# Kernel optimization log

Hardware: AMD Instinct MI355X
Metric: run time of the kernel (lower is better)

Reference implementation:

```python
import jax, jax.numpy as jnp
import numpy as np

N = 4096        # nodes
IN_DIM = 256    # input feature dim
HID = 64        # hidden per head (num_hidden_layers)
HEADS = 8
OUT_DIM = 64
ALPHA = 0.2     # LeakyReLU negative slope
NEG_INF = jnp.float32(-9e15)


def setup_inputs() -> dict:
    key = jax.random.key(0)
    ks = jax.random.split(key, 8)
    x = jax.random.normal(ks[0], (N, IN_DIM), dtype=jnp.float32)
    adj = (jax.random.uniform(ks[1], (N, N)) < 0.002).astype(jnp.float32)
    adj = jnp.maximum(adj, jnp.eye(N, dtype=jnp.float32))
    s = 0.1
    W_h = jax.random.normal(ks[2], (HEADS, IN_DIM, HID), dtype=jnp.float32) * s
    a1_h = jax.random.normal(ks[3], (HEADS, HID), dtype=jnp.float32) * s
    a2_h = jax.random.normal(ks[4], (HEADS, HID), dtype=jnp.float32) * s
    W_o = jax.random.normal(ks[5], (HEADS * HID, OUT_DIM), dtype=jnp.float32) * s
    a1_o = jax.random.normal(ks[6], (OUT_DIM,), dtype=jnp.float32) * s
    a2_o = jax.random.normal(ks[7], (OUT_DIM,), dtype=jnp.float32) * s
    return dict(x=x, adj=adj, W_h=W_h, a1_h=a1_h, a2_h=a2_h, W_o=W_o, a1_o=a1_o, a2_o=a2_o)


def _gat_heads(x, adj, W, a1, a2):
    """Multi-head GAT layer. x:[N,F], adj:[N,N], W:[H,F,O], a1/a2:[H,O] -> [H,N,O]."""
    Wh = jnp.einsum('nf,hfo->hno', x, W)                      # [H,N,O]
    f1 = jnp.einsum('hno,ho->hn', Wh, a1)                     # source scores
    f2 = jnp.einsum('hno,ho->hn', Wh, a2)                     # target scores
    e = jax.nn.leaky_relu(f1[:, :, None] + f2[:, None, :], ALPHA)  # [H,N,N]
    e = jnp.where(adj[None] > 0, e, NEG_INF)
    attn = jax.nn.softmax(e, axis=-1)                         # segment-softmax over neighbors
    return jnp.einsum('hnm,hmo->hno', attn, Wh)


def reference(x, adj, W_h, a1_h, a2_h, W_o, a1_o, a2_o):
    # dropout p=0.0 -> identity (deterministic reference)
    h = _gat_heads(x, adj, W_h, a1_h, a2_h)                   # [H,N,HID]
    h = jnp.transpose(h, (1, 0, 2)).reshape(N, HEADS * HID)   # concat heads on dim=-1
    out = _gat_heads(h, adj, W_o[None], a1_o[None], a2_o[None])[0]  # [N,OUT_DIM]
    return jax.nn.elu(out)
```

## Files before the change

kernel.cpp:

```cpp
#include <hip/hip_runtime.h>
#include <cstdint>
#include <cstddef>

#define N_NODES 4096
#define IN_DIM 256
#define HID 64
#define HEADS 8
#define OUT_DIM 64
#define ALPHA 0.2f
#define MAXDEG 64
#define TILE 16

typedef __attribute__((ext_vector_type(8))) short bf16x8;
typedef __attribute__((ext_vector_type(4))) float f32x4;

__device__ __forceinline__ unsigned short f2bf(float f) {
    unsigned u = __float_as_uint(f);
    u += 0x7fffu + ((u >> 16) & 1u);
    return (unsigned short)(u >> 16);
}
__device__ __forceinline__ float bf2f(unsigned short u) {
    return __uint_as_float(((unsigned)u) << 16);
}

__global__ __launch_bounds__(256) void k1_gemm_csr(const float* __restrict__ x,
                                                   const float* __restrict__ W,
                                                   const float* __restrict__ a1,
                                                   const float* __restrict__ a2,
                                                   unsigned short* __restrict__ Whb,
                                                   float* __restrict__ f1,
                                                   float* __restrict__ f2,
                                                   const float* __restrict__ adj,
                                                   int* __restrict__ degs,
                                                   int* __restrict__ cols) {
    __shared__ __attribute__((aligned(16))) unsigned short axs[64][72];
    __shared__ __attribute__((aligned(16))) unsigned short bws[64][72];
    int bid = blockIdx.x;
    int t = threadIdx.x;
    int w = t >> 6, l = t & 63;
    if (bid % 9 == 0) {
        int g = bid / 9;
        int h = g & 7;
        int n0 = (g >> 3) * 64;
        int m0 = (w >> 1) * 32;
        int np = (w & 1) * 32;
        f32x4 zf = {0.f, 0.f, 0.f, 0.f};
        f32x4 acc[2][2] = {{zf, zf}, {zf, zf}};
        const float4* x4 = (const float4*)x;
        const float4* w4 = (const float4*)(W + (size_t)h * IN_DIM * HID);
        for (int kc = 0; kc < IN_DIM; kc += 64) {
            __syncthreads();
            #pragma unroll
            for (int i = 0; i < 4; ++i) {
                int e = t + i * 256;
                int r = e >> 4, c4 = e & 15;
                float4 v = x4[(size_t)(n0 + r) * (IN_DIM / 4) + (kc >> 2) + c4];
                ushort4 u;
                u.x = f2bf(v.x); u.y = f2bf(v.y); u.z = f2bf(v.z); u.w = f2bf(v.w);
                *(ushort4*)&axs[r][c4 * 4] = u;
            }
            #pragma unroll
            for (int i = 0; i < 4; ++i) {
                int e = t + i * 256;
                int kk = e >> 4, c4 = e & 15;
                float4 v = w4[(size_t)(kc + kk) * (HID / 4) + c4];
                bws[4 * c4 + 0][kk] = f2bf(v.x);
                bws[4 * c4 + 1][kk] = f2bf(v.y);
                bws[4 * c4 + 2][kk] = f2bf(v.z);
                bws[4 * c4 + 3][kk] = f2bf(v.w);
            }
            __syncthreads();
            #pragma unroll
            for (int k0 = 0; k0 < 64; k0 += 32) {
                bf16x8 af[2], bfr[2];
                #pragma unroll
                for (int m = 0; m < 2; ++m)
                    af[m] = *(const bf16x8*)&axs[m0 + m * 16 + (l & 15)][k0 + (l >> 4) * 8];
                #pragma unroll
                for (int n = 0; n < 2; ++n)
                    bfr[n] = *(const bf16x8*)&bws[np + n * 16 + (l & 15)][k0 + (l >> 4) * 8];
                #pragma unroll
                for (int m = 0; m < 2; ++m)
                    #pragma unroll
                    for (int n = 0; n < 2; ++n)
                        acc[m][n] = __builtin_amdgcn_mfma_f32_16x16x32_bf16(af[m], bfr[n], acc[m][n], 0, 0, 0);
            }
        }
        __syncthreads();
        float a1c[2], a2c[2];
        #pragma unroll
        for (int n = 0; n < 2; ++n) {
            a1c[n] = a1[h * HID + np + n * 16 + (l & 15)];
            a2c[n] = a2[h * HID + np + n * 16 + (l & 15)];
        }
        float* fred = (float*)&axs[0][0];
        int wn = w & 1;
        #pragma unroll
        for (int m = 0; m < 2; ++m) {
            #pragma unroll
            for (int r = 0; r < 4; ++r) {
                int row = m0 + m * 16 + (l >> 4) * 4 + r;
                #pragma unroll
                for (int n = 0; n < 2; ++n)
                    Whb[((size_t)(n0 + row) * HEADS + h) * HID + np + n * 16 + (l & 15)] =
                        f2bf(acc[m][n][r]);
                float s1 = acc[m][0][r] * a1c[0] + acc[m][1][r] * a1c[1];
                float s2 = acc[m][0][r] * a2c[0] + acc[m][1][r] * a2c[1];
                #pragma unroll
                for (int off = 8; off; off >>= 1) {
                    s1 += __shfl_xor(s1, off);
                    s2 += __shfl_xor(s2, off);
                }
                if ((l & 15) == 0) {
                    fred[0 * 128 + wn * 64 + row] = s1;
                    fred[1 * 128 + wn * 64 + row] = s2;
                }
            }
        }
        __syncthreads();
        if (t < 64) {
            f1[(size_t)(n0 + t) * HEADS + h] = fred[t] + fred[64 + t];
            f2[(size_t)(n0 + t) * HEADS + h] = fred[128 + t] + fred[192 + t];
        }
    } else {
        int g = bid / 9, r9 = bid % 9;
        int row = g * 8 + r9 - 1;
        int* wcols = (int*)&axs[0][0];
        int* wcnt  = (int*)&bws[0][0];
        const float4* arow = (const float4*)(adj + (size_t)row * N_NODES);
        float4 v0 = arow[w * 256 + 0 * 64 + l];
        float4 v1 = arow[w * 256 + 1 * 64 + l];
        float4 v2 = arow[w * 256 + 2 * 64 + l];
        float4 v3 = arow[w * 256 + 3 * 64 + l];
        int base = 0;
        float4 vv[4] = {v0, v1, v2, v3};
        #pragma unroll
        for (int i = 0; i < 4; ++i) {
            float comp[4] = {vv[i].x, vv[i].y, vv[i].z, vv[i].w};
            #pragma unroll
            for (int q = 0; q < 4; ++q) {
                bool pred = comp[q] > 0.f;
                unsigned long long mask = __ballot(pred);
                if (pred) {
                    int pos = base + __popcll(mask & ((1ull << l) - 1ull));
                    if (pos < MAXDEG) wcols[w * MAXDEG + pos] = (w * 256 + i * 64 + l) * 4 + q;
                }
                base += __popcll(mask);
            }
        }
        if (l == 0) wcnt[w] = base < MAXDEG ? base : MAXDEG;
        __syncthreads();
        int c0 = wcnt[0], c1 = wcnt[1], c2 = wcnt[2], c3 = wcnt[3];
        int off = (w > 0 ? c0 : 0) + (w > 1 ? c1 : 0) + (w > 2 ? c2 : 0);
        int mycnt = wcnt[w];
        if (l < mycnt) {
            int gpos = off + l;
            if (gpos < MAXDEG) cols[row * MAXDEG + gpos] = wcols[w * MAXDEG + l];
        }
        if (t == 0) {
            int tot = c0 + c1 + c2 + c3;
            degs[row] = tot < MAXDEG ? tot : MAXDEG;
        }
    }
}

__global__ __launch_bounds__(256) void attn1_gemm2(const unsigned short* __restrict__ Whb,
                                                   const float* __restrict__ f1,
                                                   const float* __restrict__ f2,
                                                   const int* __restrict__ degs,
                                                   const int* __restrict__ cols,
                                                   const float* __restrict__ Wo,
                                                   const float* __restrict__ a1,
                                                   const float* __restrict__ a2,
                                                   float* __restrict__ Wh2,
                                                   float* __restrict__ f1o,
                                                   float* __restrict__ f2o) {
    __shared__ int   cols_s[TILE][MAXDEG];
    __shared__ int   deg_s[TILE];
    __shared__ float p_s[TILE][HEADS][MAXDEG];
    __shared__ __attribute__((aligned(16))) unsigned short htile[TILE][520];
    __shared__ __attribute__((aligned(16))) unsigned short bws[64][136];
    __shared__ float fred[2][4][TILE];

    int n0 = blockIdx.x * TILE;
    int t = threadIdx.x;
    int w = t >> 6, l = t & 63;

    if (t < TILE) deg_s[t] = degs[n0 + t];
    {
        int nl = t >> 4, ix = t & 15;
        #pragma unroll
        for (int it = 0; it < 4; ++it)
            cols_s[nl][ix + it * 16] = cols[(size_t)(n0 + nl) * MAXDEG + ix + it * 16];
    }
    __syncthreads();

    if (t < TILE * HEADS) {
        int nl = t >> 3, h = t & 7;
        int n = n0 + nl;
        int deg = deg_s[nl];
        float f1v = f1[n * HEADS + h];
        float m = -1e30f;
        for (int j = 0; j < deg; ++j) {
            int c = cols_s[nl][j];
            float v = f1v + f2[c * HEADS + h];
            v = v > 0.f ? v : ALPHA * v;
            p_s[nl][h][j] = v;
            m = fmaxf(m, v);
        }
        float s = 0.f;
        for (int j = 0; j < deg; ++j) {
            float p = expf(p_s[nl][h][j] - m);
            p_s[nl][h][j] = p;
            s += p;
        }
        float inv = 1.f / s;
        for (int j = 0; j < deg; ++j) p_s[nl][h][j] *= inv;
    }
    __syncthreads();

    {
        int nl = t >> 4, s16 = t & 15;
        int deg = deg_s[nl];
        float acc[4][8] = {};
        const uint4* whp = (const uint4*)Whb;
        for (int j = 0; j < deg; ++j) {
            int c = cols_s[nl][j];
            uint4 u[4];
            #pragma unroll
            for (int it = 0; it < 4; ++it)
                u[it] = whp[(size_t)c * 64 + it * 16 + s16];
            float pj[4];
            #pragma unroll
            for (int it = 0; it < 4; ++it) pj[it] = p_s[nl][it * 2 + (s16 >> 3)][j];
            #pragma unroll
            for (int it = 0; it < 4; ++it) {
                const unsigned short* up = (const unsigned short*)&u[it];
                #pragma unroll
                for (int q = 0; q < 8; ++q)
                    acc[it][q] += pj[it] * bf2f(up[q]);
            }
        }
        #pragma unroll
        for (int it = 0; it < 4; ++it) {
            unsigned short ov[8];
            #pragma unroll
            for (int q = 0; q < 8; ++q) ov[q] = f2bf(acc[it][q]);
            *(uint4*)&htile[nl][it * 128 + s16 * 8] = *(const uint4*)ov;
        }
    }

    f32x4 gacc = {0.f, 0.f, 0.f, 0.f};
    const float4* wo4 = (const float4*)Wo;
    int nbase = w * 16;
    for (int kc = 0; kc < HEADS * HID; kc += 128) {
        __syncthreads();
        #pragma unroll
        for (int i = 0; i < 8; ++i) {
            int e = t + i * 256;
            int kk = e >> 4, c4 = e & 15;
            float4 v = wo4[(size_t)(kc + kk) * (OUT_DIM / 4) + c4];
            bws[4 * c4 + 0][kk] = f2bf(v.x);
            bws[4 * c4 + 1][kk] = f2bf(v.y);
            bws[4 * c4 + 2][kk] = f2bf(v.z);
            bws[4 * c4 + 3][kk] = f2bf(v.w);
        }
        __syncthreads();
        #pragma unroll
        for (int k0 = 0; k0 < 128; k0 += 32) {
            bf16x8 af = *(const bf16x8*)&htile[l & 15][kc + k0 + (l >> 4) * 8];
            bf16x8 bfr = *(const bf16x8*)&bws[nbase + (l & 15)][k0 + (l >> 4) * 8];
            gacc = __builtin_amdgcn_mfma_f32_16x16x32_bf16(af, bfr, gacc, 0, 0, 0);
        }
    }
    float a1c = a1[nbase + (l & 15)];
    float a2c = a2[nbase + (l & 15)];
    #pragma unroll
    for (int r = 0; r < 4; ++r) {
        int row = (l >> 4) * 4 + r;
        Wh2[(size_t)(n0 + row) * OUT_DIM + nbase + (l & 15)] = gacc[r];
        float s1 = gacc[r] * a1c;
        float s2 = gacc[r] * a2c;
        #pragma unroll
        for (int off = 8; off; off >>= 1) {
            s1 += __shfl_xor(s1, off);
            s2 += __shfl_xor(s2, off);
        }
        if ((l & 15) == 0) {
            fred[0][w][row] = s1;
            fred[1][w][row] = s2;
        }
    }
    __syncthreads();
    if (t < TILE) {
        f1o[n0 + t] = fred[0][0][t] + fred[0][1][t] + fred[0][2][t] + fred[0][3][t];
        f2o[n0 + t] = fred[1][0][t] + fred[1][1][t] + fred[1][2][t] + fred[1][3][t];
    }
}

__global__ __launch_bounds__(256) void attn2(const float* __restrict__ Wh,
                                             const float* __restrict__ f1,
                                             const float* __restrict__ f2,
                                             const int* __restrict__ degs,
                                             const int* __restrict__ cols,
                                             float* __restrict__ out) {
    int wave = threadIdx.x >> 6;
    int lane = threadIdx.x & 63;
    int n = blockIdx.x * 4 + wave;
    if (n >= N_NODES) return;
    int deg = degs[n];
    int col = 0;
    float e = -1e30f;
    if (lane < deg) {
        col = cols[n * MAXDEG + lane];
        float v = f1[n] + f2[col];
        e = v > 0.f ? v : ALPHA * v;
    }
    float m = e;
    #pragma unroll
    for (int off = 32; off; off >>= 1) m = fmaxf(m, __shfl_xor(m, off));
    float p = (lane < deg) ? expf(e - m) : 0.f;
    float s = p;
    #pragma unroll
    for (int off = 32; off; off >>= 1) s += __shfl_xor(s, off);
    float inv = 1.f / s;
    float acc = 0.f;
    int j = 0;
    for (; j + 8 <= deg; j += 8) {
        int cj[8]; float pj[8]; float v[8];
        #pragma unroll
        for (int q = 0; q < 8; ++q) cj[q] = __shfl(col, j + q);
        #pragma unroll
        for (int q = 0; q < 8; ++q) pj[q] = __shfl(p, j + q);
        #pragma unroll
        for (int q = 0; q < 8; ++q) v[q] = Wh[(size_t)cj[q] * OUT_DIM + lane];
        #pragma unroll
        for (int q = 0; q < 8; ++q) acc += pj[q] * v[q];
    }
    for (; j < deg; ++j) {
        int cj = __shfl(col, j);
        float pj = __shfl(p, j);
        acc += pj * Wh[(size_t)cj * OUT_DIM + lane];
    }
    acc *= inv;
    acc = acc > 0.f ? acc : expf(acc) - 1.f;
    out[(size_t)n * OUT_DIM + lane] = acc;
}

extern "C" void kernel_launch(void* const* d_in, const int* in_sizes, int n_in,
                              void* d_out, int out_size, void* d_ws, size_t ws_size,
                              hipStream_t stream) {
    const float* x    = (const float*)d_in[0];
    const float* adj  = (const float*)d_in[1];
    const float* W_h  = (const float*)d_in[2];
    const float* a1_h = (const float*)d_in[3];
    const float* a2_h = (const float*)d_in[4];
    const float* W_o  = (const float*)d_in[5];
    const float* a1_o = (const float*)d_in[6];
    const float* a2_o = (const float*)d_in[7];
    float* out = (float*)d_out;

    float* wsf  = (float*)d_ws;
    float* Wh2  = wsf;
    float* f1_1 = Wh2 + (size_t)N_NODES * OUT_DIM;
    float* f2_1 = f1_1 + (size_t)N_NODES * HEADS;
    float* f1_2 = f2_1 + (size_t)N_NODES * HEADS;
    float* f2_2 = f1_2 + N_NODES;
    int*   degs = (int*)(f2_2 + N_NODES);
    int*   csr  = degs + N_NODES;
    unsigned short* Whb = (unsigned short*)(csr + (size_t)N_NODES * MAXDEG);

    k1_gemm_csr<<<4608, 256, 0, stream>>>(x, W_h, a1_h, a2_h, Whb, f1_1, f2_1, adj, degs, csr);

    attn1_gemm2<<<N_NODES / TILE, 256, 0, stream>>>(Whb, f1_1, f2_1, degs, csr,
                                                    W_o, a1_o, a2_o, Wh2, f1_2, f2_2);

    attn2<<<N_NODES / 4, 256, 0, stream>>>(Wh2, f1_2, f2_2, degs, csr, out);
}
```

Baseline: 53.07 us.

## Halve attn1 tile, pretranspose Wo to bf16 in k1, unroll neighbor loop

Moves the Wo fp32-to-bf16 transpose into 32 extra blocks of the first kernel, so each attn1 block copies ready bf16 rows into LDS instead of converting and scattering per block. The attn1 tile drops from 16 to 8 nodes, doubling the block count to 512 for better CU occupancy. The 8 padding rows of the MFMA A tile are zeroed and their outputs masked. The neighbor aggregation now uses 32 threads per node and unrolls two neighbors per iteration to raise memory-level parallelism. The cost is that each block reloads the full WoT for half as many nodes.

```diff
diff --git a/kernel.cpp b/kernel.cpp
--- a/kernel.cpp
+++ b/kernel.cpp
@@ -9,7 +9,7 @@
 #define OUT_DIM 64
 #define ALPHA 0.2f
 #define MAXDEG 64
-#define TILE 16
+#define TILE 8
 
 typedef __attribute__((ext_vector_type(8))) short bf16x8;
 typedef __attribute__((ext_vector_type(4))) float f32x4;
@@ -32,12 +32,25 @@
                                                    float* __restrict__ f2,
                                                    const float* __restrict__ adj,
                                                    int* __restrict__ degs,
-                                                   int* __restrict__ cols) {
+                                                   int* __restrict__ cols,
+                                                   const float* __restrict__ Wo,
+                                                   unsigned short* __restrict__ WoT) {
     __shared__ __attribute__((aligned(16))) unsigned short axs[64][72];
     __shared__ __attribute__((aligned(16))) unsigned short bws[64][72];
     int bid = blockIdx.x;
     int t = threadIdx.x;
     int w = t >> 6, l = t & 63;
+    if (bid >= 4608) {
+        int k0 = (bid - 4608) * 16;
+        #pragma unroll
+        for (int i = 0; i < 4; ++i) {
+            int e = t + i * 256;
+            int kk = k0 + (e >> 6);
+            int o = e & 63;
+            WoT[(size_t)o * 512 + kk] = f2bf(Wo[(size_t)kk * OUT_DIM + o]);
+        }
+        return;
+    }
     if (bid % 9 == 0) {
         int g = bid / 9;
         int h = g & 7;
@@ -169,7 +182,7 @@
                                                    const float* __restrict__ f2,
                                                    const int* __restrict__ degs,
                                                    const int* __restrict__ cols,
-                                                   const float* __restrict__ Wo,
+                                                   const unsigned short* __restrict__ WoT,
                                                    const float* __restrict__ a1,
                                                    const float* __restrict__ a2,
                                                    float* __restrict__ Wh2,
@@ -178,7 +191,7 @@
     __shared__ int   cols_s[TILE][MAXDEG];
     __shared__ int   deg_s[TILE];
     __shared__ float p_s[TILE][HEADS][MAXDEG];
-    __shared__ __attribute__((aligned(16))) unsigned short htile[TILE][520];
+    __shared__ __attribute__((aligned(16))) unsigned short htile[16][520];
     __shared__ __attribute__((aligned(16))) unsigned short bws[64][136];
     __shared__ float fred[2][4][TILE];
 
@@ -188,22 +201,29 @@
 
     if (t < TILE) deg_s[t] = degs[n0 + t];
     {
-        int nl = t >> 4, ix = t & 15;
-        #pragma unroll
-        for (int it = 0; it < 4; ++it)
-            cols_s[nl][ix + it * 16] = cols[(size_t)(n0 + nl) * MAXDEG + ix + it * 16];
+        int nl = t >> 5, ix = t & 31;
+        cols_s[nl][ix]      = cols[(size_t)(n0 + nl) * MAXDEG + ix];
+        cols_s[nl][ix + 32] = cols[(size_t)(n0 + nl) * MAXDEG + ix + 32];
+    }
+    {
+        uint4 z = {0u, 0u, 0u, 0u};
+        #pragma unroll
+        for (int i = 0; i < 2; ++i) {
+            int e = t + i * 256;
+            int r = 8 + (e >> 6), c8 = e & 63;
+            *(uint4*)&htile[r][c8 * 8] = z;
+        }
     }
     __syncthreads();
 
     if (t < TILE * HEADS) {
         int nl = t >> 3, h = t & 7;
-        int n = n0 + nl;
         int deg = deg_s[nl];
-        float f1v = f1[n * HEADS + h];
+        float f1v = f1[(size_t)(n0 + nl) * HEADS + h];
         float m = -1e30f;
         for (int j = 0; j < deg; ++j) {
             int c = cols_s[nl][j];
-            float v = f1v + f2[c * HEADS + h];
+            float v = f1v + f2[(size_t)c * HEADS + h];
             v = v > 0.f ? v : ALPHA * v;
             p_s[nl][h][j] = v;
             m = fmaxf(m, v);
@@ -220,50 +240,59 @@
     __syncthreads();
 
     {
-        int nl = t >> 4, s16 = t & 15;
+        int nl = t >> 5, s = t & 31;
         int deg = deg_s[nl];
-        float acc[4][8] = {};
+        int hA = s >> 3, hB = 4 + (s >> 3);
+        float accA[8] = {}, accB[8] = {};
         const uint4* whp = (const uint4*)Whb;
-        for (int j = 0; j < deg; ++j) {
-            int c = cols_s[nl][j];
-            uint4 u[4];
-            #pragma unroll
-            for (int it = 0; it < 4; ++it)
-                u[it] = whp[(size_t)c * 64 + it * 16 + s16];
-            float pj[4];
-            #pragma unroll
-            for (int it = 0; it < 4; ++it) pj[it] = p_s[nl][it * 2 + (s16 >> 3)][j];
-            #pragma unroll
-            for (int it = 0; it < 4; ++it) {
-                const unsigned short* up = (const unsigned short*)&u[it];
-                #pragma unroll
-                for (int q = 0; q < 8; ++q)
-                    acc[it][q] += pj[it] * bf2f(up[q]);
-            }
-        }
-        #pragma unroll
-        for (int it = 0; it < 4; ++it) {
-            unsigned short ov[8];
-            #pragma unroll
-            for (int q = 0; q < 8; ++q) ov[q] = f2bf(acc[it][q]);
-            *(uint4*)&htile[nl][it * 128 + s16 * 8] = *(const uint4*)ov;
-        }
+        int j = 0;
+        for (; j + 2 <= deg; j += 2) {
+            int c0 = cols_s[nl][j], c1 = cols_s[nl][j + 1];
+            uint4 u0a = whp[(size_t)c0 * 64 + s];
+            uint4 u0b = whp[(size_t)c0 * 64 + 32 + s];
+            uint4 u1a = whp[(size_t)c1 * 64 + s];
+            uint4 u1b = whp[(size_t)c1 * 64 + 32 + s];
+            float p0a = p_s[nl][hA][j],     p0b = p_s[nl][hB][j];
+            float p1a = p_s[nl][hA][j + 1], p1b = p_s[nl][hB][j + 1];
+            const unsigned short* w0a = (const unsigned short*)&u0a;
+            const unsigned short* w0b = (const unsigned short*)&u0b;
+            const unsigned short* w1a = (const unsigned short*)&u1a;
+            const unsigned short* w1b = (const unsigned short*)&u1b;
+            #pragma unroll
+            for (int q = 0; q < 8; ++q) {
+                accA[q] += p0a * bf2f(w0a[q]) + p1a * bf2f(w1a[q]);
+                accB[q] += p0b * bf2f(w0b[q]) + p1b * bf2f(w1b[q]);
+            }
+        }
+        if (j < deg) {
+            int c0 = cols_s[nl][j];
+            uint4 u0a = whp[(size_t)c0 * 64 + s];
+            uint4 u0b = whp[(size_t)c0 * 64 + 32 + s];
+            float p0a = p_s[nl][hA][j], p0b = p_s[nl][hB][j];
+            const unsigned short* w0a = (const unsigned short*)&u0a;
+            const unsigned short* w0b = (const unsigned short*)&u0b;
+            #pragma unroll
+            for (int q = 0; q < 8; ++q) {
+                accA[q] += p0a * bf2f(w0a[q]);
+                accB[q] += p0b * bf2f(w0b[q]);
+            }
+        }
+        unsigned short ovA[8], ovB[8];
+        #pragma unroll
+        for (int q = 0; q < 8; ++q) { ovA[q] = f2bf(accA[q]); ovB[q] = f2bf(accB[q]); }
+        *(uint4*)&htile[nl][s * 8]       = *(const uint4*)ovA;
+        *(uint4*)&htile[nl][256 + s * 8] = *(const uint4*)ovB;
     }
 
     f32x4 gacc = {0.f, 0.f, 0.f, 0.f};
-    const float4* wo4 = (const float4*)Wo;
     int nbase = w * 16;
     for (int kc = 0; kc < HEADS * HID; kc += 128) {
         __syncthreads();
         #pragma unroll
-        for (int i = 0; i < 8; ++i) {
+        for (int i = 0; i < 4; ++i) {
             int e = t + i * 256;
-            int kk = e >> 4, c4 = e & 15;
-            float4 v = wo4[(size_t)(kc + kk) * (OUT_DIM / 4) + c4];
-            bws[4 * c4 + 0][kk] = f2bf(v.x);
-            bws[4 * c4 + 1][kk] = f2bf(v.y);
-            bws[4 * c4 + 2][kk] = f2bf(v.z);
-            bws[4 * c4 + 3][kk] = f2bf(v.w);
+            int o = e >> 4, c8 = e & 15;
+            *(uint4*)&bws[o][c8 * 8] = *(const uint4*)&WoT[(size_t)o * 512 + kc + c8 * 8];
         }
         __syncthreads();
         #pragma unroll
@@ -278,7 +307,6 @@
     #pragma unroll
     for (int r = 0; r < 4; ++r) {
         int row = (l >> 4) * 4 + r;
-        Wh2[(size_t)(n0 + row) * OUT_DIM + nbase + (l & 15)] = gacc[r];
         float s1 = gacc[r] * a1c;
         float s2 = gacc[r] * a2c;
         #pragma unroll
@@ -286,9 +314,12 @@
             s1 += __shfl_xor(s1, off);
             s2 += __shfl_xor(s2, off);
         }
-        if ((l & 15) == 0) {
-            fred[0][w][row] = s1;
-            fred[1][w][row] = s2;
+        if (row < TILE) {
+            Wh2[(size_t)(n0 + row) * OUT_DIM + nbase + (l & 15)] = gacc[r];
+            if ((l & 15) == 0) {
+                fred[0][w][row] = s1;
+                fred[1][w][row] = s2;
+            }
         }
     }
     __syncthreads();
@@ -369,11 +400,13 @@
     int*   degs = (int*)(f2_2 + N_NODES);
     int*   csr  = degs + N_NODES;
     unsigned short* Whb = (unsigned short*)(csr + (size_t)N_NODES * MAXDEG);
-
-    k1_gemm_csr<<<4608, 256, 0, stream>>>(x, W_h, a1_h, a2_h, Whb, f1_1, f2_1, adj, degs, csr);
+    unsigned short* WoT = Whb + (size_t)N_NODES * HEADS * HID;
+
+    k1_gemm_csr<<<4640, 256, 0, stream>>>(x, W_h, a1_h, a2_h, Whb, f1_1, f2_1,
+                                          adj, degs, csr, W_o, WoT);
 
     attn1_gemm2<<<N_NODES / TILE, 256, 0, stream>>>(Whb, f1_1, f2_1, degs, csr,
-                                                    W_o, a1_o, a2_o, Wh2, f1_2, f2_2);
+                                                    WoT, a1_o, a2_o, Wh2, f1_2, f2_2);
 
     attn2<<<N_NODES / 4, 256, 0, stream>>>(Wh2, f1_2, f2_2, degs, csr, out);
 }
```

Result: faster. 48.85 us (-8.0%).
